# Optimization experiments

Measured on AMD Instinct MI355X. Metric: run time of the kernel, lower is better.

The kernel has to match this reference:

```python
import jax, jax.numpy as jnp
import numpy as np

K = 20
EPS = 1e-5  # BatchNorm eps
SLOPE = 0.2  # LeakyReLU negative slope


def _lrelu(y):
    return jnp.where(y > 0, y, SLOPE * y)


def _knn_idx(x):
    # x: [B, C, N] -> idx [B, N, K] of nearest neighbors (largest of negative sq dist)
    inner = -2.0 * jnp.einsum('bcn,bcm->bnm', x, x)
    xx = jnp.sum(x * x, axis=1)  # [B, N]
    pd = -xx[:, :, None] - inner - xx[:, None, :]  # [B, N, N]
    return jax.lax.top_k(pd, K)[1]


def _graph_feature(x):
    # x: [B, C, N] -> [B, 2C, N, K] = cat(neighbor - center, center)
    idx = _knn_idx(x)
    xt = jnp.transpose(x, (0, 2, 1))  # [B, N, C]
    nb = jax.vmap(lambda f, i: f[i])(xt, idx)  # [B, N, K, C]
    ctr = xt[:, :, None, :]
    feat = jnp.concatenate([nb - ctr, jnp.broadcast_to(ctr, nb.shape)], axis=-1)
    return jnp.transpose(feat, (0, 3, 1, 2))


def _bn(y, p, ch_axis):
    g, b, m, v = p[0], p[1], p[2], p[3]
    shape = [1] * y.ndim
    shape[ch_axis] = -1
    scale = (g / jnp.sqrt(v + EPS)).reshape(shape)
    return (y - m.reshape(shape)) * scale + b.reshape(shape)


def _conv_block(x, w, bn):
    f = _graph_feature(x)  # [B, 2C_in, N, K]
    y = jnp.einsum('bcnk,oc->bonk', f, w)  # 1x1 conv, no bias
    y = _lrelu(_bn(y, bn, 1))
    return jnp.max(y, axis=-1)  # max over K neighbors -> [B, C_out, N]


def setup_inputs() -> dict:
    key = jax.random.key(0)
    ks = jax.random.split(key, 20)
    B, N = 8, 1024
    inp = {
        'x': jax.random.normal(ks[0], (B, 3, N), jnp.float32),
        'w0': jax.random.normal(ks[1], (64, 6), jnp.float32) * 0.1,
        'w1': jax.random.normal(ks[2], (64, 128), jnp.float32) * 0.1,
        'w2': jax.random.normal(ks[3], (128, 128), jnp.float32) * 0.1,
        'w3': jax.random.normal(ks[4], (256, 256), jnp.float32) * 0.1,
        'bn0': jax.random.uniform(ks[5], (4, 64), jnp.float32) + 0.1,
        'bn1': jax.random.uniform(ks[6], (4, 64), jnp.float32) + 0.1,
        'bn2': jax.random.uniform(ks[7], (4, 128), jnp.float32) + 0.1,
        'bn3': jax.random.uniform(ks[8], (4, 256), jnp.float32) + 0.1,
        'we': jax.random.normal(ks[9], (1024, 512), jnp.float32) * 0.05,
        'bne': jax.random.uniform(ks[10], (4, 1024), jnp.float32) + 0.1,
        'wf0': jax.random.normal(ks[11], (512, 2048), jnp.float32) * 0.02,
        'bnf0': jax.random.uniform(ks[12], (4, 512), jnp.float32) + 0.1,
        'wf1': jax.random.normal(ks[13], (256, 512), jnp.float32) * 0.05,
        'bnf1': jax.random.uniform(ks[14], (4, 256), jnp.float32) + 0.1,
        'wfin': jax.random.normal(ks[15], (64, 256), jnp.float32) * 0.05,
        'bfin': jax.random.normal(ks[16], (64,), jnp.float32) * 0.05,
    }
    return inp


def reference(x, w0, w1, w2, w3, bn0, bn1, bn2, bn3, we, bne, wf0, bnf0, wf1, bnf1, wfin, bfin):
    B = x.shape[0]
    x1 = _conv_block(x, w0, bn0)   # [B, 64, N]
    x2 = _conv_block(x1, w1, bn1)  # [B, 64, N]
    x3 = _conv_block(x2, w2, bn2)  # [B, 128, N]
    x4 = _conv_block(x3, w3, bn3)  # [B, 256, N]
    cat = jnp.concatenate([x1, x2, x3, x4], axis=1)  # [B, 512, N]
    e = _lrelu(_bn(jnp.einsum('bcn,oc->bon', cat, we), bne, 1))  # [B, 1024, N]
    p1 = jnp.max(e, axis=-1)
    p2 = jnp.mean(e, axis=-1)
    h = jnp.concatenate([p1, p2], axis=1)  # [B, 2048]
    h = _lrelu(_bn(h @ wf0.T, bnf0, 1))  # [B, 512]; dropout is eval-mode identity
    h = _lrelu(_bn(h @ wf1.T, bnf1, 1))  # [B, 256]
    return h @ wfin.T + bfin  # [B, 64]
```

## Files before the change

### kernel.cpp

```cpp
#include <hip/hip_runtime.h>
#include <math.h>

#define N_PTS 1024
#define BATCH 8
#define KNN 20
#define EPSB 1e-5f
#define SLOPE 0.2f

typedef __attribute__((ext_vector_type(8))) short short8;
typedef __attribute__((ext_vector_type(4))) float f32x4;
typedef unsigned short ushort_t;
typedef unsigned long long u64;

__device__ __forceinline__ float lrelu(float y) { return y > 0.f ? y : SLOPE * y; }

__device__ __forceinline__ ushort_t f2bf(float f) {
    union { float f; unsigned u; } v; v.f = f;
    unsigned r = v.u + 0x7FFF + ((v.u >> 16) & 1);
    return (ushort_t)(r >> 16);
}

__device__ __forceinline__ void wprep_one(const float* __restrict__ w, float* __restrict__ wpt,
                                          int C, int Cout, int g) {
    int M2 = 2 * Cout;
    if (g >= C * M2) return;
    int c = g / M2, m = g - c * M2;
    float v;
    if (m < Cout) v = w[(size_t)m * 2 * C + c];
    else { int o = m - Cout; v = w[(size_t)o * 2 * C + C + c] - w[(size_t)o * 2 * C + c]; }
    wpt[(size_t)c * M2 + m] = v;
}

__global__ void prep_kernel(const float* __restrict__ we, ushort_t* __restrict__ weh,
                            const float* __restrict__ w0, float* __restrict__ wpt0,
                            const float* __restrict__ w1, float* __restrict__ wpt1,
                            const float* __restrict__ w2, float* __restrict__ wpt2,
                            const float* __restrict__ w3, float* __restrict__ wpt3) {
    int bx = blockIdx.x, tid = threadIdx.x;
    if (bx < 512) {
        int g = bx * 256 + tid;
        float4 v = ((const float4*)we)[g];
        ushort4 o;
        o.x = f2bf(v.x); o.y = f2bf(v.y); o.z = f2bf(v.z); o.w = f2bf(v.w);
        ((ushort4*)weh)[g] = o;
    } else if (bx < 514) {
        wprep_one(w0, wpt0, 3, 64, (bx - 512) * 256 + tid);
    } else if (bx < 546) {
        wprep_one(w1, wpt1, 64, 64, (bx - 514) * 256 + tid);
    } else if (bx < 610) {
        wprep_one(w2, wpt2, 64, 128, (bx - 546) * 256 + tid);
    } else {
        wprep_one(w3, wpt3, 128, 256, (bx - 610) * 256 + tid);
    }
}

__global__ void __launch_bounds__(256)
pdabv_kernel(const float* __restrict__ x, const float* __restrict__ wpt,
             float* __restrict__ pd, float* __restrict__ A, float* __restrict__ Bv,
             int C, int Cout, int bstride) {
    int b = blockIdx.z;
    int nt = blockIdx.y;
    int bx = blockIdx.x;
    int tid = threadIdx.x;
    int tx = tid & 15, ty = tid >> 4;
    int n0 = nt * 128;
    __shared__ float sU0[16][128];
    __shared__ float sU1[16][128];
    __shared__ float sXX[256];
    const float* xb = x + (size_t)b * bstride;
    float acc[8][8] = {};
    if (bx < 8) {
        int m0 = bx * 128;
        float xxa = 0.f;
        for (int c0 = 0; c0 < C; c0 += 16) {
            for (int q = 0; q < 2; q++) {
                int f = q * 256 + tid;
                int r = f >> 5, col = (f & 31) * 4;
                int c = c0 + r;
                float4 vn = {0.f, 0.f, 0.f, 0.f}, vm = {0.f, 0.f, 0.f, 0.f};
                if (c < C) {
                    vn = *(const float4*)&xb[(size_t)c * N_PTS + n0 + col];
                    vm = *(const float4*)&xb[(size_t)c * N_PTS + m0 + col];
                }
                *(float4*)&sU0[r][col] = vn;
                *(float4*)&sU1[r][col] = vm;
            }
            __syncthreads();
            if (tid < 128) {
                for (int k = 0; k < 16; k++) { float v = sU0[k][tid]; xxa += v * v; }
            } else {
                int u = tid - 128;
                for (int k = 0; k < 16; k++) { float v = sU1[k][u]; xxa += v * v; }
            }
            for (int k = 0; k < 16; k++) {
                float4 a0 = *(const float4*)&sU0[k][ty * 4];
                float4 a1 = *(const float4*)&sU0[k][64 + ty * 4];
                float4 b0 = *(const float4*)&sU1[k][tx * 4];
                float4 b1 = *(const float4*)&sU1[k][64 + tx * 4];
                float av[8] = {a0.x, a0.y, a0.z, a0.w, a1.x, a1.y, a1.z, a1.w};
                float bw[8] = {b0.x, b0.y, b0.z, b0.w, b1.x, b1.y, b1.z, b1.w};
                for (int i = 0; i < 8; i++)
                    for (int j = 0; j < 8; j++) acc[i][j] += av[i] * bw[j];
            }
            __syncthreads();
        }
        sXX[tid] = xxa;
        __syncthreads();
        float xnv[8], xmv[8];
        for (int i = 0; i < 8; i++) xnv[i] = sXX[(i >> 2) * 64 + ty * 4 + (i & 3)];
        for (int j = 0; j < 8; j++) xmv[j] = sXX[128 + (j >> 2) * 64 + tx * 4 + (j & 3)];
        for (int i = 0; i < 8; i++) {
            int n = n0 + (i >> 2) * 64 + ty * 4 + (i & 3);
            float* prow = pd + ((size_t)(b * N_PTS + n)) * N_PTS;
            for (int jh = 0; jh < 2; jh++) {
                float4 o;
                o.x = 2.f * acc[i][jh * 4 + 0] - xnv[i] - xmv[jh * 4 + 0];
                o.y = 2.f * acc[i][jh * 4 + 1] - xnv[i] - xmv[jh * 4 + 1];
                o.z = 2.f * acc[i][jh * 4 + 2] - xnv[i] - xmv[jh * 4 + 2];
                o.w = 2.f * acc[i][jh * 4 + 3] - xnv[i] - xmv[jh * 4 + 3];
                *(float4*)&prow[m0 + jh * 64 + tx * 4] = o;
            }
        }
    } else {
        int m0 = (bx - 8) * 128;
        int M2 = 2 * Cout;
        for (int c0 = 0; c0 < C; c0 += 16) {
            for (int q = 0; q < 2; q++) {
                int f = q * 256 + tid;
                int r = f >> 5, col = (f & 31) * 4;
                int c = c0 + r;
                float4 vw = {0.f, 0.f, 0.f, 0.f}, vx = {0.f, 0.f, 0.f, 0.f};
                if (c < C) {
                    vw = *(const float4*)&wpt[(size_t)c * M2 + m0 + col];
                    vx = *(const float4*)&xb[(size_t)c * N_PTS + n0 + col];
                }
                *(float4*)&sU0[r][col] = vw;
                *(float4*)&sU1[r][col] = vx;
            }
            __syncthreads();
            for (int k = 0; k < 16; k++) {
                float4 a0 = *(const float4*)&sU0[k][ty * 4];
                float4 a1 = *(const float4*)&sU0[k][64 + ty * 4];
                float4 b0 = *(const float4*)&sU1[k][tx * 4];
                float4 b1 = *(const float4*)&sU1[k][64 + tx * 4];
                float av[8] = {a0.x, a0.y, a0.z, a0.w, a1.x, a1.y, a1.z, a1.w};
                float bw[8] = {b0.x, b0.y, b0.z, b0.w, b1.x, b1.y, b1.z, b1.w};
                for (int i = 0; i < 8; i++)
                    for (int j = 0; j < 8; j++) acc[i][j] += av[i] * bw[j];
            }
            __syncthreads();
        }
        for (int i = 0; i < 8; i++) {
            int rowm = m0 + (i >> 2) * 64 + ty * 4 + (i & 3);
            float* dst = (rowm < Cout) ? (A + ((size_t)b * Cout + rowm) * N_PTS)
                                       : (Bv + ((size_t)b * Cout + rowm - Cout) * N_PTS);
            for (int jh = 0; jh < 2; jh++) {
                float4 o;
                o.x = acc[i][jh * 4 + 0];
                o.y = acc[i][jh * 4 + 1];
                o.z = acc[i][jh * 4 + 2];
                o.w = acc[i][jh * 4 + 3];
                *(float4*)&dst[n0 + jh * 64 + tx * 4] = o;
            }
        }
    }
}

__global__ void __launch_bounds__(256)
topk_kernel(const float* __restrict__ pd, int* __restrict__ idx) {
    int wid = threadIdx.x >> 6;
    int row = blockIdx.x * 4 + wid;
    int lane = threadIdx.x & 63;
    __shared__ u64 Sk[4][64];
    const float* p = pd + (size_t)row * N_PTS;
    float v[16];
    for (int q = 0; q < 4; q++) {
        float4 t = *(const float4*)&p[lane * 16 + q * 4];
        v[q * 4 + 0] = t.x; v[q * 4 + 1] = t.y; v[q * 4 + 2] = t.z; v[q * 4 + 3] = t.w;
    }
    float lmax = v[0];
    #pragma unroll
    for (int j = 1; j < 16; j++) lmax = fmaxf(lmax, v[j]);
    float s = lmax;
    #pragma unroll
    for (int k = 2; k <= 64; k <<= 1) {
        #pragma unroll
        for (int j = k >> 1; j > 0; j >>= 1) {
            float o = __shfl_xor(s, j, 64);
            bool takeMin = (((lane & k) == 0) == ((lane & j) == 0));
            float mn = fminf(s, o), mx = fmaxf(s, o);
            s = takeMin ? mn : mx;
        }
    }
    float tp = __shfl(s, 44, 64);
    unsigned hm = 0;
    #pragma unroll
    for (int j = 0; j < 16; j++) hm |= (v[j] >= tp ? 1u : 0u) << j;
    int cnt = __popc(hm);
    int incl = cnt;
    #pragma unroll
    for (int d = 1; d < 64; d <<= 1) {
        int o = __shfl_up(incl, d, 64);
        if (lane >= d) incl += o;
    }
    int total = __shfl(incl, 63, 64);
    int pos = incl - cnt;
    if (total <= 64) {
        #pragma unroll
        for (int j = 0; j < 16; j++) {
            if (hm & (1u << j)) {
                unsigned u = __float_as_uint(v[j]);
                unsigned msk = ((unsigned)((int)u >> 31)) | 0x80000000u;
                Sk[wid][pos] = ((u64)(u ^ msk) << 32) | (unsigned)(1023 - (lane * 16 + j));
                pos++;
            }
        }
        u64 key = (lane < total) ? Sk[wid][lane] : 0ull;
        #pragma unroll
        for (int k = 2; k <= 64; k <<= 1) {
            #pragma unroll
            for (int j = k >> 1; j > 0; j >>= 1) {
                u64 o = __shfl_xor(key, j, 64);
                bool takeMin = (((lane & k) == 0) == ((lane & j) == 0));
                bool sgt = key > o;
                key = (sgt != takeMin) ? key : o;
            }
        }
        if (lane >= 44) {
            int m = 1023 - (int)(unsigned)(key & 0xFFFFFFFFu);
            idx[row * KNN + (63 - lane)] = m;
        }
    } else {
        for (int kk = 0; kk < KNN; kk++) {
            float bv = v[0]; int bj = 0;
            #pragma unroll
            for (int j = 1; j < 16; j++) if (v[j] > bv) { bv = v[j]; bj = j; }
            int bi = lane * 16 + bj;
            for (int d = 32; d > 0; d >>= 1) {
                float ov = __shfl_down(bv, d, 64);
                int oi = __shfl_down(bi, d, 64);
                if (ov > bv || (ov == bv && oi < bi)) { bv = ov; bi = oi; }
            }
            bi = __shfl(bi, 0, 64);
            if ((bi >> 4) == lane) {
                #pragma unroll
                for (int j = 0; j < 16; j++) if (j == (bi & 15)) v[j] = -INFINITY;
            }
            if (lane == 0) idx[row * KNN + kk] = bi;
        }
    }
}

__global__ void __launch_bounds__(256)
gmax_kernel(const float* __restrict__ A, const float* __restrict__ Bv,
            const int* __restrict__ idx, const float* __restrict__ bnp,
            float* __restrict__ out, int Cout, int outStrideB) {
    int b = blockIdx.z;
    int n0 = blockIdx.x * 64;
    int o0 = blockIdx.y * 4;
    int tid = threadIdx.x;
    __shared__ int sidx[64 * 21];
    __shared__ float sA[4][N_PTS];
    for (int t = tid; t < 64 * KNN; t += 256) {
        int nl = t / KNN, k = t - nl * KNN;
        sidx[nl * 21 + k] = idx[(b * N_PTS + n0) * KNN + t];
    }
    const float* Abase = A + ((size_t)b * Cout + o0) * N_PTS;
    for (int q = 0; q < 4; q++) {
        int f = q * 256 + tid;
        int r = f >> 8, c4 = (f & 255) * 4;
        *(float4*)&sA[r][c4] = *(const float4*)&Abase[(size_t)r * N_PTS + c4];
    }
    __syncthreads();
    int nl = tid & 63, ol = tid >> 6;
    float best = -INFINITY;
    #pragma unroll
    for (int k = 0; k < KNN; k++) {
        int j = sidx[nl * 21 + k];
        best = fmaxf(best, sA[ol][j]);
    }
    int o = o0 + ol;
    int n = n0 + nl;
    float pre = best + Bv[((size_t)b * Cout + o) * N_PTS + n];
    float g = bnp[o], bb = bnp[Cout + o], m = bnp[2 * Cout + o], vv = bnp[3 * Cout + o];
    float scale = g / sqrtf(vv + EPSB);
    out[(size_t)b * outStrideB + (size_t)o * N_PTS + n] = lrelu((pre - m) * scale + bb);
}

__global__ void catT_kernel(const float* __restrict__ cat, ushort_t* __restrict__ catT) {
    int b = blockIdx.z, ct = blockIdx.y, nt = blockIdx.x;
    int tid = threadIdx.x;
    __shared__ float tile[64][65];
    const float* cb = cat + (size_t)b * 512 * N_PTS;
    for (int q = 0; q < 16; q++) {
        int e = q * 256 + tid;
        int c = e >> 6, n = e & 63;
        tile[c][n] = cb[(size_t)(ct * 64 + c) * N_PTS + nt * 64 + n];
    }
    __syncthreads();
    for (int q = 0; q < 16; q++) {
        int e = q * 256 + tid;
        int n = e >> 6, c = e & 63;
        catT[((size_t)b * N_PTS + nt * 64 + n) * 512 + ct * 64 + c] = f2bf(tile[c][n]);
    }
}

__global__ void __launch_bounds__(256)
gemm6_mfma(const ushort_t* __restrict__ weh, const ushort_t* __restrict__ catT,
           const float* __restrict__ bne,
           float* __restrict__ pmax, float* __restrict__ psum) {
    int b = blockIdx.z, ot = blockIdx.y, nt = blockIdx.x;
    int tid = threadIdx.x;
    int w = tid >> 6, lane = tid & 63, q = lane >> 4, lr = lane & 15;
    int mblk = w >> 1, nblk = w & 1;
    __shared__ __align__(16) ushort_t sA[128 * 40];
    __shared__ __align__(16) ushort_t sB[128 * 40];
    __shared__ float sa[128], sc[128];
    __shared__ float redmax[128][2], redsum[128][2];
    int o0 = ot * 128, n0 = nt * 128;
    if (tid < 128) {
        int o = o0 + tid;
        float g = bne[o], bb = bne[1024 + o], m = bne[2048 + o], vv = bne[3072 + o];
        float scale = g / sqrtf(vv + EPSB);
        sa[tid] = scale; sc[tid] = bb - m * scale;
    }
    f32x4 acc[4][4] = {};
    const ushort_t* cT = catT + (size_t)b * N_PTS * 512;
    int r0 = tid >> 2, s = tid & 3;
    for (int k0 = 0; k0 < 512; k0 += 32) {
        __syncthreads();
        for (int h = 0; h < 2; h++) {
            int r = r0 + h * 64;
            *(short8*)&sA[r * 40 + s * 8] = *(const short8*)(weh + (size_t)(o0 + r) * 512 + k0 + s * 8);
            *(short8*)&sB[r * 40 + s * 8] = *(const short8*)(cT  + (size_t)(n0 + r) * 512 + k0 + s * 8);
        }
        __syncthreads();
        short8 af[4], bfr[4];
        for (int mi = 0; mi < 4; mi++)
            af[mi] = *(const short8*)&sA[(mblk * 64 + mi * 16 + lr) * 40 + q * 8];
        for (int ni = 0; ni < 4; ni++)
            bfr[ni] = *(const short8*)&sB[(nblk * 64 + ni * 16 + lr) * 40 + q * 8];
        for (int mi = 0; mi < 4; mi++)
            for (int ni = 0; ni < 4; ni++)
                acc[mi][ni] = __builtin_amdgcn_mfma_f32_16x16x32_bf16(af[mi], bfr[ni], acc[mi][ni], 0, 0, 0);
    }
    for (int mi = 0; mi < 4; mi++) {
        for (int r = 0; r < 4; r++) {
            int row = mblk * 64 + mi * 16 + q * 4 + r;
            float a = sa[row], c = sc[row];
            float mx = -INFINITY, sm = 0.f;
            for (int ni = 0; ni < 4; ni++) {
                float y = lrelu(acc[mi][ni][r] * a + c);
                mx = fmaxf(mx, y); sm += y;
            }
            for (int msk = 1; msk < 16; msk <<= 1) {
                mx = fmaxf(mx, __shfl_xor(mx, msk, 16));
                sm += __shfl_xor(sm, msk, 16);
            }
            if (lr == 0) { redmax[row][nblk] = mx; redsum[row][nblk] = sm; }
        }
    }
    __syncthreads();
    if (tid < 128) {
        float mx = fmaxf(redmax[tid][0], redmax[tid][1]);
        float sm = redsum[tid][0] + redsum[tid][1];
        int o = o0 + tid;
        pmax[((size_t)(b * 1024 + o)) * 8 + nt] = mx;
        psum[((size_t)(b * 1024 + o)) * 8 + nt] = sm;
    }
}

__global__ void pool_reduce_kernel(const float* __restrict__ pmax, const float* __restrict__ psum,
                                   float* __restrict__ h0) {
    int g = blockIdx.x * 256 + threadIdx.x;
    int b = g >> 10, o = g & 1023;
    float mx = -INFINITY, sm = 0.f;
    for (int t = 0; t < 8; t++) { mx = fmaxf(mx, pmax[g * 8 + t]); sm += psum[g * 8 + t]; }
    h0[(size_t)b * 2048 + o] = mx;
    h0[(size_t)b * 2048 + 1024 + o] = sm * (1.0f / 1024.0f);
}

__global__ void fc_kernel(const float* __restrict__ in, const float* __restrict__ w,
                          const float* __restrict__ bnp, const float* __restrict__ bias,
                          float* __restrict__ out, int Cin, int Cout, int mode) {
    int blk = blockIdx.x;
    int b = blk / Cout, o = blk % Cout;
    int lane = threadIdx.x;
    const float* inb = in + (size_t)b * Cin;
    const float* wo = w + (size_t)o * Cin;
    float acc = 0.f;
    for (int c = lane; c < Cin; c += 64) acc += inb[c] * wo[c];
    for (int s = 32; s > 0; s >>= 1) acc += __shfl_down(acc, s, 64);
    if (lane == 0) {
        float y = acc;
        if (mode == 0) {
            float g = bnp[o], bb = bnp[Cout + o], m = bnp[2 * Cout + o], vv = bnp[3 * Cout + o];
            y = lrelu((y - m) * (g / sqrtf(vv + EPSB)) + bb);
        } else {
            y += bias[o];
        }
        out[(size_t)b * Cout + o] = y;
    }
}

extern "C" void kernel_launch(void* const* d_in, const int* in_sizes, int n_in,
                              void* d_out, int out_size, void* d_ws, size_t ws_size,
                              hipStream_t stream) {
    const float* x    = (const float*)d_in[0];
    const float* w0   = (const float*)d_in[1];
    const float* w1   = (const float*)d_in[2];
    const float* w2   = (const float*)d_in[3];
    const float* w3   = (const float*)d_in[4];
    const float* bn0  = (const float*)d_in[5];
    const float* bn1  = (const float*)d_in[6];
    const float* bn2  = (const float*)d_in[7];
    const float* bn3  = (const float*)d_in[8];
    const float* we   = (const float*)d_in[9];
    const float* bne  = (const float*)d_in[10];
    const float* wf0  = (const float*)d_in[11];
    const float* bnf0 = (const float*)d_in[12];
    const float* wf1  = (const float*)d_in[13];
    const float* bnf1 = (const float*)d_in[14];
    const float* wfin = (const float*)d_in[15];
    const float* bfin = (const float*)d_in[16];

    float* ws = (float*)d_ws;
    size_t off = 0;
    float* cat  = ws + off; off += (size_t)BATCH * 512 * N_PTS;
    float* pd   = ws + off; off += (size_t)BATCH * N_PTS * N_PTS;
    float* A    = ws + off; off += (size_t)BATCH * 256 * N_PTS;
    float* Bv   = ws + off; off += (size_t)BATCH * 256 * N_PTS;
    float* pmax = ws + off; off += (size_t)BATCH * N_PTS * 8;
    float* psum = ws + off; off += (size_t)BATCH * N_PTS * 8;
    float* h0   = ws + off; off += (size_t)BATCH * 2048;
    float* h1   = ws + off; off += (size_t)BATCH * 512;
    float* h2   = ws + off; off += (size_t)BATCH * 256;
    int*   idx  = (int*)(ws + off); off += (size_t)BATCH * N_PTS * KNN;
    ushort_t* weh  = (ushort_t*)(ws + off); off += (size_t)(1024 * 512) / 2;
    ushort_t* catT = (ushort_t*)(ws + off); off += (size_t)BATCH * N_PTS * 512 / 2;
    float* wpt0 = ws + off; off += 3 * 128;
    float* wpt1 = ws + off; off += 64 * 128;
    float* wpt2 = ws + off; off += 64 * 256;
    float* wpt3 = ws + off; off += 128 * 512;

    const int CSTR = 512 * N_PTS;
    const int topkBlocks = BATCH * N_PTS / 4;

    prep_kernel<<<866, 256, 0, stream>>>(we, weh, w0, wpt0, w1, wpt1, w2, wpt2, w3, wpt3);

    pdabv_kernel<<<dim3(9, 8, BATCH), 256, 0, stream>>>(x, wpt0, pd, A, Bv, 3, 64, 3 * N_PTS);
    topk_kernel<<<topkBlocks, 256, 0, stream>>>(pd, idx);
    gmax_kernel<<<dim3(16, 16, BATCH), 256, 0, stream>>>(A, Bv, idx, bn0, cat, 64, CSTR);

    pdabv_kernel<<<dim3(9, 8, BATCH), 256, 0, stream>>>(cat, wpt1, pd, A, Bv, 64, 64, CSTR);
    topk_kernel<<<topkBlocks, 256, 0, stream>>>(pd, idx);
    gmax_kernel<<<dim3(16, 16, BATCH), 256, 0, stream>>>(A, Bv, idx, bn1, cat + 64 * N_PTS, 64, CSTR);

    pdabv_kernel<<<dim3(10, 8, BATCH), 256, 0, stream>>>(cat + 64 * N_PTS, wpt2, pd, A, Bv, 64, 128, CSTR);
    topk_kernel<<<topkBlocks, 256, 0, stream>>>(pd, idx);
    gmax_kernel<<<dim3(16, 32, BATCH), 256, 0, stream>>>(A, Bv, idx, bn2, cat + 128 * N_PTS, 128, CSTR);

    pdabv_kernel<<<dim3(12, 8, BATCH), 256, 0, stream>>>(cat + 128 * N_PTS, wpt3, pd, A, Bv, 128, 256, CSTR);
    topk_kernel<<<topkBlocks, 256, 0, stream>>>(pd, idx);
    gmax_kernel<<<dim3(16, 64, BATCH), 256, 0, stream>>>(A, Bv, idx, bn3, cat + 256 * N_PTS, 256, CSTR);

    catT_kernel<<<dim3(16, 8, BATCH), 256, 0, stream>>>(cat, catT);
    gemm6_mfma<<<dim3(8, 8, BATCH), 256, 0, stream>>>(weh, catT, bne, pmax, psum);
    pool_reduce_kernel<<<32, 256, 0, stream>>>(pmax, psum, h0);

    fc_kernel<<<BATCH * 512, 64, 0, stream>>>(h0, wf0, bnf0, nullptr, h1, 2048, 512, 0);
    fc_kernel<<<BATCH * 256, 64, 0, stream>>>(h1, wf1, bnf1, nullptr, h2, 512, 256, 0);
    fc_kernel<<<BATCH * 64, 64, 0, stream>>>(h2, wfin, nullptr, bfin, (float*)d_out, 256, 64, 1);
}
```

Baseline: 331.1 us.

## Use bf16x3-split MFMA for pairwise-distance and edge-conv projection GEMMs

Replaces the FP32 VALU pairwise-distance/projection kernel for layers 1-3 with an MFMA bf16 kernel. Inputs and weights are split into three bf16 terms (hi/mid/lo) and six cross-product passes, which approximates FP32 accuracy. A new split_kernel transposes the activations, performs the split, and computes squared norms. The aim is to move the O(N^2 C) inner-product work onto matrix cores. The cost is an extra launch and staging buffer per layer, six times the K-dimension work, and possible small precision differences that could change neighbor selection.

```diff
diff --git a/kernel.cpp b/kernel.cpp
--- a/kernel.cpp
+++ b/kernel.cpp
@@ -18,6 +18,9 @@
     union { float f; unsigned u; } v; v.f = f;
     unsigned r = v.u + 0x7FFF + ((v.u >> 16) & 1);
     return (ushort_t)(r >> 16);
+}
+__device__ __forceinline__ float bf2f(ushort_t h) {
+    union { unsigned u; float f; } v; v.u = ((unsigned)h) << 16; return v.f;
 }
 
 __device__ __forceinline__ void wprep_one(const float* __restrict__ w, float* __restrict__ wpt,
@@ -31,11 +34,27 @@
     wpt[(size_t)c * M2 + m] = v;
 }
 
+__device__ __forceinline__ void wext_one(const float* __restrict__ w, ushort_t* __restrict__ Wext,
+                                         int C, int Cout, int g, int lg2C) {
+    int M2 = 2 * Cout;
+    if (g >= C * M2) return;
+    int m = g >> lg2C, c = g & (C - 1);
+    float v;
+    if (m < Cout) v = w[(size_t)m * 2 * C + c];
+    else { int o = m - Cout; v = w[(size_t)o * 2 * C + C + c] - w[(size_t)o * 2 * C + c]; }
+    ushort_t h = f2bf(v);
+    float r1 = v - bf2f(h);
+    ushort_t md = f2bf(r1);
+    ushort_t lo = f2bf(r1 - bf2f(md));
+    ushort_t* dst = Wext + (size_t)m * 3 * C + c;
+    dst[0] = h; dst[C] = md; dst[2 * C] = lo;
+}
+
 __global__ void prep_kernel(const float* __restrict__ we, ushort_t* __restrict__ weh,
                             const float* __restrict__ w0, float* __restrict__ wpt0,
-                            const float* __restrict__ w1, float* __restrict__ wpt1,
-                            const float* __restrict__ w2, float* __restrict__ wpt2,
-                            const float* __restrict__ w3, float* __restrict__ wpt3) {
+                            const float* __restrict__ w1, ushort_t* __restrict__ Wext1,
+                            const float* __restrict__ w2, ushort_t* __restrict__ Wext2,
+                            const float* __restrict__ w3, ushort_t* __restrict__ Wext3) {
     int bx = blockIdx.x, tid = threadIdx.x;
     if (bx < 512) {
         int g = bx * 256 + tid;
@@ -46,18 +65,123 @@
     } else if (bx < 514) {
         wprep_one(w0, wpt0, 3, 64, (bx - 512) * 256 + tid);
     } else if (bx < 546) {
-        wprep_one(w1, wpt1, 64, 64, (bx - 514) * 256 + tid);
+        wext_one(w1, Wext1, 64, 64, (bx - 514) * 256 + tid, 6);
     } else if (bx < 610) {
-        wprep_one(w2, wpt2, 64, 128, (bx - 546) * 256 + tid);
+        wext_one(w2, Wext2, 64, 128, (bx - 546) * 256 + tid, 6);
     } else {
-        wprep_one(w3, wpt3, 128, 256, (bx - 610) * 256 + tid);
+        wext_one(w3, Wext3, 128, 256, (bx - 610) * 256 + tid, 7);
     }
 }
 
 __global__ void __launch_bounds__(256)
-pdabv_kernel(const float* __restrict__ x, const float* __restrict__ wpt,
-             float* __restrict__ pd, float* __restrict__ A, float* __restrict__ Bv,
-             int C, int Cout, int bstride) {
+split_kernel(const float* __restrict__ in, ushort_t* __restrict__ xT3,
+             float* __restrict__ xxv, int C, int bstride) {
+    int b = blockIdx.z, nt = blockIdx.x;
+    int tid = threadIdx.x;
+    __shared__ float tile[64][65];
+    const float* ib = in + (size_t)b * bstride;
+    int S3 = 3 * C;
+    float xxa = 0.f;
+    for (int ct = 0; ct < C; ct += 64) {
+        __syncthreads();
+        for (int qq = 0; qq < 16; qq++) {
+            int e = qq * 256 + tid;
+            int c = e >> 6, n = e & 63;
+            tile[c][n] = ib[(size_t)(ct + c) * N_PTS + nt * 64 + n];
+        }
+        __syncthreads();
+        if (tid < 64) {
+            for (int c = 0; c < 64; c++) { float v = tile[c][tid]; xxa += v * v; }
+        }
+        for (int qq = 0; qq < 16; qq++) {
+            int e = qq * 256 + tid;
+            int n = e >> 6, c = e & 63;
+            float v = tile[c][n];
+            ushort_t h = f2bf(v);
+            float r1 = v - bf2f(h);
+            ushort_t md = f2bf(r1);
+            ushort_t lo = f2bf(r1 - bf2f(md));
+            ushort_t* dst = xT3 + ((size_t)b * N_PTS + nt * 64 + n) * S3 + ct + c;
+            dst[0] = h; dst[C] = md; dst[2 * C] = lo;
+        }
+    }
+    if (tid < 64) xxv[b * N_PTS + nt * 64 + tid] = xxa;
+}
+
+__global__ void __launch_bounds__(256)
+pdabv_mfma(const ushort_t* __restrict__ xT3, const ushort_t* __restrict__ Wext,
+           const float* __restrict__ xxv,
+           float* __restrict__ pd, float* __restrict__ A, float* __restrict__ Bv,
+           int C, int lg2C, int Cout) {
+    int b = blockIdx.z, mt = blockIdx.y, nt = blockIdx.x;
+    int tid = threadIdx.x;
+    int w = tid >> 6, lane = tid & 63, q = lane >> 4, lr = lane & 15;
+    int mblk = w >> 1, nblk = w & 1;
+    const int S3 = 3 * C;
+    bool isPd = (mt < 8);
+    const ushort_t* Abase = isPd ? (xT3 + ((size_t)b * N_PTS + mt * 128) * S3)
+                                 : (Wext + (size_t)(mt - 8) * 128 * S3);
+    const ushort_t* Bbase = xT3 + ((size_t)b * N_PTS + nt * 128) * S3;
+    __shared__ __align__(16) ushort_t sA[128 * 40];
+    __shared__ __align__(16) ushort_t sB[128 * 40];
+    __shared__ float sxxA[128], sxxB[128];
+    if (isPd && tid < 128) {
+        sxxA[tid] = xxv[b * N_PTS + mt * 128 + tid];
+        sxxB[tid] = xxv[b * N_PTS + nt * 128 + tid];
+    }
+    f32x4 acc[4][4] = {};
+    int r0 = tid >> 2, s = tid & 3;
+    const int pA[6] = {0, 0, 1, 1, 0, 2};
+    const int pB[6] = {0, 1, 0, 1, 2, 0};
+    for (int ks = 0; ks < 6 * C; ks += 32) {
+        int seg = ks >> lg2C;
+        int kl = ks & (C - 1);
+        int aoff = pA[seg] * C + kl, boff = pB[seg] * C + kl;
+        __syncthreads();
+        for (int h = 0; h < 2; h++) {
+            int r = r0 + h * 64;
+            *(short8*)&sA[r * 40 + s * 8] = *(const short8*)(Abase + (size_t)r * S3 + aoff + s * 8);
+            *(short8*)&sB[r * 40 + s * 8] = *(const short8*)(Bbase + (size_t)r * S3 + boff + s * 8);
+        }
+        __syncthreads();
+        short8 af[4], bfr[4];
+        for (int mi = 0; mi < 4; mi++)
+            af[mi] = *(const short8*)&sA[(mblk * 64 + mi * 16 + lr) * 40 + q * 8];
+        for (int ni = 0; ni < 4; ni++)
+            bfr[ni] = *(const short8*)&sB[(nblk * 64 + ni * 16 + lr) * 40 + q * 8];
+        for (int mi = 0; mi < 4; mi++)
+            for (int ni = 0; ni < 4; ni++)
+                acc[mi][ni] = __builtin_amdgcn_mfma_f32_16x16x32_bf16(af[mi], bfr[ni], acc[mi][ni], 0, 0, 0);
+    }
+    if (isPd) {
+        for (int mi = 0; mi < 4; mi++)
+        for (int r = 0; r < 4; r++) {
+            int row = mblk * 64 + mi * 16 + q * 4 + r;
+            float xr = sxxA[row];
+            float* prow = pd + ((size_t)(b * N_PTS + mt * 128 + row)) * N_PTS + nt * 128;
+            for (int ni = 0; ni < 4; ni++) {
+                int col = nblk * 64 + ni * 16 + lr;
+                prow[col] = 2.f * acc[mi][ni][r] - xr - sxxB[col];
+            }
+        }
+    } else {
+        for (int mi = 0; mi < 4; mi++)
+        for (int r = 0; r < 4; r++) {
+            int rowm = (mt - 8) * 128 + mblk * 64 + mi * 16 + q * 4 + r;
+            float* dst = (rowm < Cout) ? (A + ((size_t)b * Cout + rowm) * N_PTS)
+                                       : (Bv + ((size_t)b * Cout + rowm - Cout) * N_PTS);
+            for (int ni = 0; ni < 4; ni++) {
+                int col = nblk * 64 + ni * 16 + lr;
+                dst[nt * 128 + col] = acc[mi][ni][r];
+            }
+        }
+    }
+}
+
+__global__ void __launch_bounds__(256)
+pdabv_valu(const float* __restrict__ x, const float* __restrict__ wpt,
+           float* __restrict__ pd, float* __restrict__ A, float* __restrict__ Bv,
+           int C, int Cout, int bstride) {
     int b = blockIdx.z;
     int nt = blockIdx.y;
     int bx = blockIdx.x;
@@ -435,32 +559,37 @@
     float* h0   = ws + off; off += (size_t)BATCH * 2048;
     float* h1   = ws + off; off += (size_t)BATCH * 512;
     float* h2   = ws + off; off += (size_t)BATCH * 256;
+    float* xxv  = ws + off; off += (size_t)BATCH * N_PTS;
     int*   idx  = (int*)(ws + off); off += (size_t)BATCH * N_PTS * KNN;
     ushort_t* weh  = (ushort_t*)(ws + off); off += (size_t)(1024 * 512) / 2;
     ushort_t* catT = (ushort_t*)(ws + off); off += (size_t)BATCH * N_PTS * 512 / 2;
+    ushort_t* xT3  = (ushort_t*)(ws + off); off += (size_t)BATCH * N_PTS * 3 * 128 / 2;
+    ushort_t* Wext1 = (ushort_t*)(ws + off); off += (size_t)(128 * 3 * 64) / 2;
+    ushort_t* Wext2 = (ushort_t*)(ws + off); off += (size_t)(256 * 3 * 64) / 2;
+    ushort_t* Wext3 = (ushort_t*)(ws + off); off += (size_t)(512 * 3 * 128) / 2;
     float* wpt0 = ws + off; off += 3 * 128;
-    float* wpt1 = ws + off; off += 64 * 128;
-    float* wpt2 = ws + off; off += 64 * 256;
-    float* wpt3 = ws + off; off += 128 * 512;
 
     const int CSTR = 512 * N_PTS;
     const int topkBlocks = BATCH * N_PTS / 4;
 
-    prep_kernel<<<866, 256, 0, stream>>>(we, weh, w0, wpt0, w1, wpt1, w2, wpt2, w3, wpt3);
-
-    pdabv_kernel<<<dim3(9, 8, BATCH), 256, 0, stream>>>(x, wpt0, pd, A, Bv, 3, 64, 3 * N_PTS);
+    prep_kernel<<<866, 256, 0, stream>>>(we, weh, w0, wpt0, w1, Wext1, w2, Wext2, w3, Wext3);
+
+    pdabv_valu<<<dim3(9, 8, BATCH), 256, 0, stream>>>(x, wpt0, pd, A, Bv, 3, 64, 3 * N_PTS);
     topk_kernel<<<topkBlocks, 256, 0, stream>>>(pd, idx);
     gmax_kernel<<<dim3(16, 16, BATCH), 256, 0, stream>>>(A, Bv, idx, bn0, cat, 64, CSTR);
 
-    pdabv_kernel<<<dim3(9, 8, BATCH), 256, 0, stream>>>(cat, wpt1, pd, A, Bv, 64, 64, CSTR);
+    split_kernel<<<dim3(16, 1, BATCH), 256, 0, stream>>>(cat, xT3, xxv, 64, CSTR);
+    pdabv_mfma<<<dim3(8, 9, BATCH), 256, 0, stream>>>(xT3, Wext1, xxv, pd, A, Bv, 64, 6, 64);
     topk_kernel<<<topkBlocks, 256, 0, stream>>>(pd, idx);
     gmax_kernel<<<dim3(16, 16, BATCH), 256, 0, stream>>>(A, Bv, idx, bn1, cat + 64 * N_PTS, 64, CSTR);
 
-    pdabv_kernel<<<dim3(10, 8, BATCH), 256, 0, stream>>>(cat + 64 * N_PTS, wpt2, pd, A, Bv, 64, 128, CSTR);
+    split_kernel<<<dim3(16, 1, BATCH), 256, 0, stream>>>(cat + 64 * N_PTS, xT3, xxv, 64, CSTR);
+    pdabv_mfma<<<dim3(8, 10, BATCH), 256, 0, stream>>>(xT3, Wext2, xxv, pd, A, Bv, 64, 6, 128);
     topk_kernel<<<topkBlocks, 256, 0, stream>>>(pd, idx);
     gmax_kernel<<<dim3(16, 32, BATCH), 256, 0, stream>>>(A, Bv, idx, bn2, cat + 128 * N_PTS, 128, CSTR);
 
-    pdabv_kernel<<<dim3(12, 8, BATCH), 256, 0, stream>>>(cat + 128 * N_PTS, wpt3, pd, A, Bv, 128, 256, CSTR);
+    split_kernel<<<dim3(16, 1, BATCH), 256, 0, stream>>>(cat + 128 * N_PTS, xT3, xxv, 128, CSTR);
+    pdabv_mfma<<<dim3(8, 12, BATCH), 256, 0, stream>>>(xT3, Wext3, xxv, pd, A, Bv, 128, 7, 256);
     topk_kernel<<<topkBlocks, 256, 0, stream>>>(pd, idx);
     gmax_kernel<<<dim3(16, 64, BATCH), 256, 0, stream>>>(A, Bv, idx, bn3, cat + 256 * N_PTS, 256, CSTR);
 
```

Result: slower. 343.2 us (+3.6%).
